# Kernel tuning notes

Hardware: AMD Instinct MI355X
Metric: run time of the kernel (lower is better)

Reference implementation:

```python
import jax, jax.numpy as jnp
import numpy as np

N, M, E, F, OUT = 20000, 2048, 320000, 512, 2
HID = F // 2
NEG_ATT = 0.2   # leaky_relu slope inside HypergraphConv attention
NEG = 0.01      # default F.leaky_relu / nn.LeakyReLU slope
EPS = 1e-5      # GraphNorm eps


def setup_inputs() -> dict:
    key = jax.random.key(0)
    ks = jax.random.split(key, 12)
    nrm = lambda k, shape, s=0.05: (jax.random.normal(k, shape, jnp.float32) * s)
    row = jax.random.randint(ks[1], (E,), 0, N)
    col = jax.random.randint(ks[2], (E,), 0, M)
    return dict(
        x=nrm(ks[0], (N, F), 1.0),
        edge_index=jnp.stack([row, col]),                 # [2, E] int32
        edge_attr=nrm(ks[3], (M, F), 1.0),
        W1=nrm(ks[4], (F, F)), att1=nrm(ks[5], (2 * F,)), b1=jnp.zeros((F,), jnp.float32),
        W2=nrm(ks[6], (F, F)), att2=nrm(ks[7], (2 * F,)), b2=jnp.zeros((F,), jnp.float32),
        gn1_w=jnp.ones((F,), jnp.float32), gn1_b=jnp.zeros((F,), jnp.float32), gn1_ms=jnp.ones((F,), jnp.float32),
        gn2_w=jnp.ones((F,), jnp.float32), gn2_b=jnp.zeros((F,), jnp.float32), gn2_ms=jnp.ones((F,), jnp.float32),
        fc1_W=nrm(ks[8], (F, HID)), fc1_b=jnp.zeros((HID,), jnp.float32),
        fc2_W=nrm(ks[9], (F, HID)), fc2_b=jnp.zeros((HID,), jnp.float32),
        cls_W=nrm(ks[10], (HID, OUT)), cls_b=jnp.zeros((OUT,), jnp.float32),
    )


def _segsum(v, idx, n):
    return jax.ops.segment_sum(v, idx, num_segments=n)


def hypergraph_conv(x, edge_attr, row, col, W, att, bias):
    """PyG HypergraphConv, heads=1, use_attention=True, attention_mode='node'."""
    xl = x @ W                          # [N, F] node features after lin
    el = edge_attr @ W                  # [M, F] hyperedge features after lin
    # attention logits per incidence: (cat[x_i, e_j] * att).sum(-1)
    pre = xl[row] @ att[:F] + el[col] @ att[F:]           # [E]
    alpha = jax.nn.leaky_relu(pre, NEG_ATT)
    # softmax grouped by hyperedge (col)
    amax = jax.ops.segment_max(alpha, col, num_segments=M)
    amax = jnp.where(jnp.isfinite(amax), amax, 0.0)
    ex = jnp.exp(alpha - amax[col])
    denom = _segsum(ex, col, M)
    alpha = ex / jnp.maximum(denom, 1e-16)[col]           # [E]
    # degree normalizations (hyperedge_weight = 1)
    ones = jnp.ones((row.shape[0],), xl.dtype)
    deg_n = _segsum(ones, row, N)
    Dinv = jnp.where(deg_n > 0, 1.0 / deg_n, 0.0)         # [N]
    deg_e = _segsum(ones, col, M)
    Binv = jnp.where(deg_e > 0, 1.0 / deg_e, 0.0)         # [M]
    # propagate 1: nodes -> hyperedges
    edge_feat = _segsum((alpha * Binv[col])[:, None] * xl[row], col, M)   # [M, F]
    # propagate 2: hyperedges -> nodes
    out = _segsum((alpha * Dinv[row])[:, None] * edge_feat[col], row, N)  # [N, F]
    return out + bias


def graph_norm(x, w, b, ms):
    # single graph (batch=None): normalize over all nodes
    mean = x.mean(axis=0)
    out = x - ms * mean
    var = (out * out).mean(axis=0)
    return out / jnp.sqrt(var + EPS) * w + b


def reference(x, edge_index, edge_attr,
              W1, att1, b1, W2, att2, b2,
              gn1_w, gn1_b, gn1_ms, gn2_w, gn2_b, gn2_ms,
              fc1_W, fc1_b, fc2_W, fc2_b, cls_W, cls_b):
    row, col = edge_index[0], edge_index[1]
    h = hypergraph_conv(x, edge_attr, row, col, W1, att1, b1)
    h = jax.nn.leaky_relu(graph_norm(h, gn1_w, gn1_b, gn1_ms), NEG)
    out = jax.nn.leaky_relu(h @ fc1_W + fc1_b, NEG)
    h = hypergraph_conv(h, edge_attr, row, col, W2, att2, b2)
    h = jax.nn.leaky_relu(graph_norm(h, gn2_w, gn2_b, gn2_ms), NEG)
    out = out + jax.nn.leaky_relu(h @ fc2_W + fc2_b, NEG)
    logits = out @ cls_W + cls_b
    return logits
```

## Files before the change

### kernel.cpp

```cpp
#include <hip/hip_runtime.h>
#include <math.h>

#define FDIM 512
#define HIDDIM 256
#define HB 128
#define SCH 1024
#define LDSK 32

typedef __bf16 bf16x8 __attribute__((ext_vector_type(8)));
typedef float floatx4 __attribute__((ext_vector_type(4)));

__device__ __forceinline__ float lrelu(float x, float s) { return x >= 0.0f ? x : s * x; }

__device__ __forceinline__ float bf2f(unsigned int u) {
  union { float f; unsigned int i; } v; v.i = u << 16; return v.f;
}
__device__ __forceinline__ unsigned short f2bf(float f) {
  union { float f; unsigned int u; } v; v.f = f;
  unsigned int x = v.u;
  return (unsigned short)((x + 0x7fffu + ((x >> 16) & 1u)) >> 16);
}

__device__ __forceinline__ void async_copy16(const unsigned short* g, unsigned short* l) {
  __builtin_amdgcn_global_load_lds((const __attribute__((address_space(1))) unsigned int*)g,
                                   (__attribute__((address_space(3))) unsigned int*)l, 16, 0, 0);
}

__device__ __forceinline__ float waveReduceSum(float v) {
#pragma unroll
  for (int o = 32; o; o >>= 1) v += __shfl_down(v, o, 64);
  return v;
}

__device__ __forceinline__ float blockReduceSum256(float v) {
  __shared__ float sm[4];
  int lane = threadIdx.x & 63, w = threadIdx.x >> 6;
  v = waveReduceSum(v);
  __syncthreads();
  if (lane == 0) sm[w] = v;
  __syncthreads();
  return sm[0] + sm[1] + sm[2] + sm[3];
}

__device__ __forceinline__ float blockReduceMax256(float v) {
  __shared__ float sm[4];
  int lane = threadIdx.x & 63, w = threadIdx.x >> 6;
#pragma unroll
  for (int o = 32; o; o >>= 1) v = fmaxf(v, __shfl_down(v, o, 64));
  __syncthreads();
  if (lane == 0) sm[w] = v;
  __syncthreads();
  return fmaxf(fmaxf(sm[0], sm[1]), fmaxf(sm[2], sm[3]));
}

__global__ __launch_bounds__(256) void k_hist2(const int* __restrict__ row, const int* __restrict__ col,
                                               int* __restrict__ cnt_r, int* __restrict__ cnt_c,
                                               int E, int nchunk) {
  __shared__ int h[2048];
  int b = blockIdx.x, t = threadIdx.x;
  for (int i = t; i < 2048; i += 256) h[i] = 0;
  __syncthreads();
  int s = b * nchunk, e = min(E, s + nchunk);
  for (int j = s + t; j < e; j += 256) {
    atomicAdd(&h[col[j]], 1);
    atomicAdd(&cnt_r[row[j]], 1);
  }
  __syncthreads();
  for (int i = t; i < 2048; i += 256) {
    int v = h[i];
    if (v) atomicAdd(&cnt_c[i], v);
  }
}

__global__ __launch_bounds__(256) void k_scan_part(const int* __restrict__ cnt, int* __restrict__ off,
                                                   int* __restrict__ btot, int n) {
  int b = blockIdx.x, t = threadIdx.x;
  int base = b * SCH + t * 4;
  int v[4];
#pragma unroll
  for (int i = 0; i < 4; ++i) v[i] = (base + i < n) ? cnt[base + i] : 0;
  int s = v[0] + v[1] + v[2] + v[3];
  int lane = t & 63, w = t >> 6;
  int x = s;
#pragma unroll
  for (int o = 1; o < 64; o <<= 1) {
    int y = __shfl_up(x, o, 64);
    if (lane >= o) x += y;
  }
  __shared__ int ws[4];
  if (lane == 63) ws[w] = x;
  __syncthreads();
  int wpre = 0;
  for (int i = 0; i < w; ++i) wpre += ws[i];
  int run = wpre + x - s;
#pragma unroll
  for (int i = 0; i < 4; ++i) {
    if (base + i < n) off[base + i] = run;
    run += v[i];
  }
  if (t == 255) btot[b] = wpre + x;
}

__global__ __launch_bounds__(256) void k_scan_midcol(int* __restrict__ btot, int nb,
                                                     const int* __restrict__ cnt_c, int* __restrict__ off_c,
                                                     int* __restrict__ gcur) {
  int t = threadIdx.x, lane = t & 63, w = t >> 6;
  __shared__ int ws[4];
  if (blockIdx.x == 0) {
    int v = (t < nb) ? btot[t] : 0;
    int x = v;
#pragma unroll
    for (int o = 1; o < 64; o <<= 1) {
      int y = __shfl_up(x, o, 64);
      if (lane >= o) x += y;
    }
    if (lane == 63) ws[w] = x;
    __syncthreads();
    int wpre = 0;
    for (int i = 0; i < w; ++i) wpre += ws[i];
    if (t < nb) btot[t] = wpre + x - v;
    if (t == 255) btot[nb] = wpre + x;
  } else {
    int base = t * 8;
    int v[8];
#pragma unroll
    for (int i = 0; i < 8; ++i) v[i] = cnt_c[base + i];
    int s = 0;
#pragma unroll
    for (int i = 0; i < 8; ++i) s += v[i];
    int x = s;
#pragma unroll
    for (int o = 1; o < 64; o <<= 1) {
      int y = __shfl_up(x, o, 64);
      if (lane >= o) x += y;
    }
    if (lane == 63) ws[w] = x;
    __syncthreads();
    int wpre = 0;
    for (int i = 0; i < w; ++i) wpre += ws[i];
    int run = wpre + x - s;
#pragma unroll
    for (int i = 0; i < 8; ++i) {
      off_c[base + i] = run;
      gcur[base + i] = run;
      run += v[i];
    }
    if (t == 255) off_c[2048] = wpre + x;
  }
}

__global__ __launch_bounds__(256) void k_scan_add(int* __restrict__ off, const int* __restrict__ btot,
                                                  int n, int nb) {
  int b = blockIdx.x, t = threadIdx.x;
  int base = b * SCH + t * 4;
  int add = btot[b];
#pragma unroll
  for (int i = 0; i < 4; ++i)
    if (base + i < n) off[base + i] += add;
  if (b == 0 && t == 0) off[n] = btot[nb];
}

__global__ __launch_bounds__(256) void k_fill3(const int* __restrict__ row, const int* __restrict__ col,
                                               int* __restrict__ gcur, const int* __restrict__ off_r,
                                               int* __restrict__ cur_r, int* __restrict__ prj,
                                               int* __restrict__ rj, int* __restrict__ cj,
                                               int E, int nchunk) {
  __shared__ int h[2048];
  __shared__ int lbase[2048];
  int b = blockIdx.x, t = threadIdx.x;
  for (int i = t; i < 2048; i += 256) h[i] = 0;
  __syncthreads();
  int s = b * nchunk, e = min(E, s + nchunk);
  for (int j = s + t; j < e; j += 256) atomicAdd(&h[col[j]], 1);
  __syncthreads();
  for (int i = t; i < 2048; i += 256) {
    int c = h[i];
    lbase[i] = c ? atomicAdd(&gcur[i], c) : 0;
    h[i] = 0;
  }
  __syncthreads();
  for (int j = s + t; j < e; j += 256) {
    int r = row[j], c = col[j];
    int slot_c = lbase[c] + atomicAdd(&h[c], 1);
    int slot_r = off_r[r] + atomicAdd(&cur_r[r], 1);
    rj[slot_c] = r;
    prj[slot_c] = slot_r;
    cj[slot_r] = c;
  }
}

__global__ __launch_bounds__(256) void k_hi(const float* __restrict__ A, unsigned short* __restrict__ hi, int n4) {
  int i = blockIdx.x * 256 + threadIdx.x;
  if (i < n4) {
    float4 v = ((const float4*)A)[i];
    ushort4 h;
    h.x = f2bf(v.x); h.y = f2bf(v.y); h.z = f2bf(v.z); h.w = f2bf(v.w);
    ((ushort4*)hi)[i] = h;
  }
}

__global__ __launch_bounds__(256) void k_prep_w_hi2(const float* __restrict__ W1, unsigned short* __restrict__ t1,
                                                    const float* __restrict__ W2, unsigned short* __restrict__ t2,
                                                    int K, int Nc) {
  const float* W = blockIdx.z ? W2 : W1;
  unsigned short* th = blockIdx.z ? t2 : t1;
  int n = blockIdx.x * 16 + (threadIdx.x & 15);
  int k = blockIdx.y * 16 + (threadIdx.x >> 4);
  th[(size_t)n * K + k] = f2bf(W[(size_t)k * Nc + n]);
}

__global__ __launch_bounds__(256) void k_prep_w2(const float* __restrict__ Wa, unsigned short* __restrict__ tha,
                                                 unsigned short* __restrict__ tla, const float* __restrict__ Wb,
                                                 unsigned short* __restrict__ thb, unsigned short* __restrict__ tlb,
                                                 int K, int Nc) {
  const float* W = blockIdx.z ? Wb : Wa;
  unsigned short* th = blockIdx.z ? thb : tha;
  unsigned short* tl = blockIdx.z ? tlb : tla;
  int n = blockIdx.x * 16 + (threadIdx.x & 15);
  int k = blockIdx.y * 16 + (threadIdx.x >> 4);
  float v = W[(size_t)k * Nc + n];
  unsigned short h = f2bf(v);
  unsigned short l = f2bf(v - bf2f(h));
  th[(size_t)n * K + k] = h;
  tl[(size_t)n * K + k] = l;
}

__global__ __launch_bounds__(256) void k_wv2(const float* __restrict__ W1, const float* __restrict__ a1,
                                             const float* __restrict__ W2, const float* __restrict__ a2,
                                             float* __restrict__ wv1, float* __restrict__ wv2) {
  int lane = threadIdx.x & 63, w = threadIdx.x >> 6;
  int k = blockIdx.x * 4 + w;
  const float* W = blockIdx.y ? W2 : W1;
  const float* a = blockIdx.y ? a2 : a1;
  float* wv = blockIdx.y ? wv2 : wv1;
  float s = 0.f;
  for (int f = lane; f < FDIM; f += 64) s = fmaf(W[(size_t)k * FDIM + f], a[f], s);
  s = waveReduceSum(s);
  if (lane == 0) wv[k] = s;
}

__global__ __launch_bounds__(256) void k_ea2(const float* __restrict__ X, const float* __restrict__ wv1,
                                             const float* __restrict__ wv2, float* __restrict__ ea1,
                                             float* __restrict__ ea2, int Mr) {
  int lane = threadIdx.x & 63, w = threadIdx.x >> 6;
  int m = blockIdx.x * 4 + w;
  if (m < Mr) {
    float s1 = 0.f, s2 = 0.f;
    for (int f = lane; f < FDIM; f += 64) {
      float v = X[(size_t)m * FDIM + f];
      s1 = fmaf(v, wv1[f], s1);
      s2 = fmaf(v, wv2[f], s2);
    }
    s1 = waveReduceSum(s1);
    s2 = waveReduceSum(s2);
    if (lane == 0) { ea1[m] = s1; ea2[m] = s2; }
  }
}

__device__ __forceinline__ bool xcd_decode(int id, int nP, int& panel, int& c) {
  panel = ((id >> 5) << 3) + (id & 7);
  c = (id >> 3) & 3;
  return panel < nP;
}

__global__ __launch_bounds__(256, 1) void gemm_conv(const unsigned short* __restrict__ Ah,
                                                    const unsigned short* __restrict__ Bth,
                                                    unsigned short* __restrict__ Cb,
                                                    const float* __restrict__ att, float* __restrict__ xa,
                                                    int Mr, int K, int Nc, int nP) {
  int panel, cblk;
  if (!xcd_decode(blockIdx.x, nP, panel, cblk)) return;
  __shared__ unsigned short lds[2 * 128 * LDSK];
  int tid = threadIdx.x, lane = tid & 63, w = tid >> 6;
  int wr = w >> 1, wc = w & 1;
  int rowB = panel * 128, colB = cblk * 128;

  const unsigned short* src = (w < 2) ? Ah : Bth;
  int baseRow = ((w < 2) ? rowB : colB) + 64 * (w & 1);
  int maxRow = (w < 2) ? (Mr - 1) : (Nc - 1);
  int slr = lane >> 2, slc = lane & 3;
  unsigned short* dstBase = &lds[((w >> 1) * 128 + (w & 1) * 64) * LDSK];

  size_t gro[4];
#pragma unroll
  for (int seg = 0; seg < 4; ++seg) {
    int rg = baseRow + seg * 16 + slr;
    if (rg > maxRow) rg = maxRow;
    gro[seg] = (size_t)rg * K + slc * 8;
  }

  floatx4 zero4 = {0.f, 0.f, 0.f, 0.f};
  floatx4 acc[4][4];
#pragma unroll
  for (int i = 0; i < 4; ++i)
#pragma unroll
    for (int j = 0; j < 4; ++j) acc[i][j] = zero4;

  int fr = lane & 15, fq = lane >> 4;
  int offA = (wr * 64 + fr) * LDSK + fq * 8;
  int offB = 128 * LDSK + (wc * 64 + fr) * LDSK + fq * 8;

  for (int k0 = 0; k0 < K; k0 += 32) {
#pragma unroll
    for (int seg = 0; seg < 4; ++seg) async_copy16(src + gro[seg] + k0, dstBase + seg * 16 * LDSK);
    __syncthreads();
    bf16x8 a[4], b[4];
#pragma unroll
    for (int t = 0; t < 4; ++t) {
      a[t] = *(const bf16x8*)(&lds[offA + t * 16 * LDSK]);
      b[t] = *(const bf16x8*)(&lds[offB + t * 16 * LDSK]);
    }
#pragma unroll
    for (int ti = 0; ti < 4; ++ti)
#pragma unroll
      for (int tj = 0; tj < 4; ++tj)
        acc[ti][tj] = __builtin_amdgcn_mfma_f32_16x16x32_bf16(a[ti], b[tj], acc[ti][tj], 0, 0, 0);
    __syncthreads();
  }

  int colL = colB + wc * 64 + fr;
  int rowL = rowB + wr * 64 + fq * 4;
  float attv[4];
#pragma unroll
  for (int tj = 0; tj < 4; ++tj) attv[tj] = att[colL + tj * 16];
#pragma unroll
  for (int ti = 0; ti < 4; ++ti) {
#pragma unroll
    for (int r = 0; r < 4; ++r) {
      int rr = rowL + ti * 16 + r;
      if (rr < Mr) {
        float dot = 0.f;
#pragma unroll
        for (int tj = 0; tj < 4; ++tj) {
          float v = acc[ti][tj][r];
          Cb[(size_t)rr * Nc + colL + tj * 16] = f2bf(v);
          dot = fmaf(v, attv[tj], dot);
        }
#pragma unroll
        for (int o = 1; o < 16; o <<= 1) dot += __shfl_xor(dot, o, 64);
        if ((lane & 15) == 0) atomicAdd(&xa[rr], dot);
      }
    }
  }
}

__global__ __launch_bounds__(256, 1) void gemm_fc_cls(const unsigned short* __restrict__ A1,
                                                      const unsigned short* __restrict__ B1h,
                                                      const unsigned short* __restrict__ B1l,
                                                      const float* __restrict__ b1,
                                                      const unsigned short* __restrict__ A2,
                                                      const unsigned short* __restrict__ B2h,
                                                      const unsigned short* __restrict__ B2l,
                                                      const float* __restrict__ b2,
                                                      const float* __restrict__ clsW, const float* __restrict__ clsb,
                                                      float* __restrict__ logits, int Mr, int K, int nP) {
  int panel, cblk;
  if (!xcd_decode(blockIdx.x, nP, panel, cblk)) return;
  __shared__ unsigned short lds[(128 + 2 * 64) * LDSK];
  int tid = threadIdx.x, lane = tid & 63, w = tid >> 6;
  int wr = w >> 1, wc = w & 1;
  int rowB = panel * 128, colB = cblk * 64;

  int slr = lane >> 2, slc = lane & 3;
  int baseRow = (w < 2) ? (rowB + 64 * w) : colB;
  int maxRow = (w < 2) ? (Mr - 1) : (HIDDIM - 1);
  unsigned short* dstBase = &lds[w * 64 * LDSK];

  size_t gro[4];
#pragma unroll
  for (int seg = 0; seg < 4; ++seg) {
    int rg = baseRow + seg * 16 + slr;
    if (rg > maxRow) rg = maxRow;
    gro[seg] = (size_t)rg * K + slc * 8;
  }

  int fr = lane & 15, fq = lane >> 4;
  int offA = (wr * 64 + fr) * LDSK + fq * 8;
  int offBh = (128 + wc * 32 + fr) * LDSK + fq * 8;
  int offBl = offBh + 64 * LDSK;

  floatx4 zero4 = {0.f, 0.f, 0.f, 0.f};
  floatx4 acc1[4][2], acc2[4][2];
#pragma unroll
  for (int i = 0; i < 4; ++i) {
    acc1[i][0] = zero4; acc1[i][1] = zero4;
    acc2[i][0] = zero4; acc2[i][1] = zero4;
  }

#pragma unroll
  for (int L = 0; L < 2; ++L) {
    const unsigned short* src =
        (L == 0) ? ((w < 2) ? A1 : (w == 2) ? B1h : B1l)
                 : ((w < 2) ? A2 : (w == 2) ? B2h : B2l);
    for (int k0 = 0; k0 < K; k0 += 32) {
#pragma unroll
      for (int seg = 0; seg < 4; ++seg) async_copy16(src + gro[seg] + k0, dstBase + seg * 16 * LDSK);
      __syncthreads();
      bf16x8 a[4], bh[2], bl[2];
#pragma unroll
      for (int t = 0; t < 4; ++t) a[t] = *(const bf16x8*)(&lds[offA + t * 16 * LDSK]);
#pragma unroll
      for (int t = 0; t < 2; ++t) {
        bh[t] = *(const bf16x8*)(&lds[offBh + t * 16 * LDSK]);
        bl[t] = *(const bf16x8*)(&lds[offBl + t * 16 * LDSK]);
      }
      if (L == 0) {
#pragma unroll
        for (int ti = 0; ti < 4; ++ti)
#pragma unroll
          for (int tj = 0; tj < 2; ++tj) {
            acc1[ti][tj] = __builtin_amdgcn_mfma_f32_16x16x32_bf16(a[ti], bh[tj], acc1[ti][tj], 0, 0, 0);
            acc1[ti][tj] = __builtin_amdgcn_mfma_f32_16x16x32_bf16(a[ti], bl[tj], acc1[ti][tj], 0, 0, 0);
          }
      } else {
#pragma unroll
        for (int ti = 0; ti < 4; ++ti)
#pragma unroll
          for (int tj = 0; tj < 2; ++tj) {
            acc2[ti][tj] = __builtin_amdgcn_mfma_f32_16x16x32_bf16(a[ti], bh[tj], acc2[ti][tj], 0, 0, 0);
            acc2[ti][tj] = __builtin_amdgcn_mfma_f32_16x16x32_bf16(a[ti], bl[tj], acc2[ti][tj], 0, 0, 0);
          }
      }
      __syncthreads();
    }
  }

  int colL = colB + wc * 32 + fr;
  int rowL = rowB + wr * 64 + fq * 4;
  float cw0[2], cw1[2], bb1[2], bb2[2];
#pragma unroll
  for (int tj = 0; tj < 2; ++tj) {
    int c = colL + tj * 16;
    cw0[tj] = clsW[2 * c];
    cw1[tj] = clsW[2 * c + 1];
    bb1[tj] = b1[c];
    bb2[tj] = b2[c];
  }
  bool addBias = (cblk == 0 && wc == 0);
  float cb0 = clsb[0], cb1 = clsb[1];
#pragma unroll
  for (int ti = 0; ti < 4; ++ti) {
#pragma unroll
    for (int r = 0; r < 4; ++r) {
      int rr = rowL + ti * 16 + r;
      if (rr < Mr) {
        float d0 = 0.f, d1 = 0.f;
#pragma unroll
        for (int tj = 0; tj < 2; ++tj) {
          float v = lrelu(acc1[ti][tj][r] + bb1[tj], 0.01f) + lrelu(acc2[ti][tj][r] + bb2[tj], 0.01f);
          d0 = fmaf(v, cw0[tj], d0);
          d1 = fmaf(v, cw1[tj], d1);
        }
#pragma unroll
        for (int o = 1; o < 16; o <<= 1) {
          d0 += __shfl_xor(d0, o, 64);
          d1 += __shfl_xor(d1, o, 64);
        }
        if ((lane & 15) == 0) {
          if (addBias) { d0 += cb0; d1 += cb1; }
          atomicAdd(&logits[2 * (size_t)rr], d0);
          atomicAdd(&logits[2 * (size_t)rr + 1], d1);
        }
      }
    }
  }
}

__global__ __launch_bounds__(256) void k_prop_col_f(const unsigned short* __restrict__ xl,
                                                    const float* __restrict__ xa, const float* __restrict__ ea,
                                                    const int* __restrict__ rj, const int* __restrict__ prj,
                                                    const int* __restrict__ off_c,
                                                    float* __restrict__ arj, unsigned short* __restrict__ ef) {
  int m = blockIdx.x;
  int s = off_c[m], e_ = off_c[m + 1];
  int cnt = e_ - s;
  float eam = ea[m];
  int t = threadIdx.x, lane = t & 63, w = t >> 6;

  __shared__ int sidx[512];
  __shared__ float swgt[512];
  __shared__ float pf[4][512];
  float acc[8] = {0, 0, 0, 0, 0, 0, 0, 0};

  if (cnt <= 512) {
    float mx = -3.402823466e38f;
    for (int j = t; j < cnt; j += 256) {
      int r = rj[s + j];
      float lg = lrelu(xa[r] + eam, 0.2f);
      sidx[j] = r;
      swgt[j] = lg;
      mx = fmaxf(mx, lg);
    }
    mx = blockReduceMax256(mx);
    float sum = 0.f;
    for (int j = t; j < cnt; j += 256) sum += expf(swgt[j] - mx);
    sum = blockReduceSum256(sum);
    float inv = 1.0f / fmaxf(sum, 1e-16f);
    for (int j = t; j < cnt; j += 256) {
      float a = expf(swgt[j] - mx) * inv;
      swgt[j] = a;
      arj[prj[s + j]] = a;
    }
    __syncthreads();
    int j = w;
    for (; j + 16 <= cnt; j += 16) {
      int r0 = sidx[j], r1 = sidx[j + 4], r2 = sidx[j + 8], r3 = sidx[j + 12];
      float w0 = swgt[j], w1 = swgt[j + 4], w2 = swgt[j + 8], w3 = swgt[j + 12];
      bf16x8 v0 = *(const bf16x8*)(xl + (size_t)r0 * FDIM + lane * 8);
      bf16x8 v1 = *(const bf16x8*)(xl + (size_t)r1 * FDIM + lane * 8);
      bf16x8 v2 = *(const bf16x8*)(xl + (size_t)r2 * FDIM + lane * 8);
      bf16x8 v3 = *(const bf16x8*)(xl + (size_t)r3 * FDIM + lane * 8);
#pragma unroll
      for (int i = 0; i < 8; ++i) acc[i] = fmaf(w0, (float)v0[i], acc[i]);
#pragma unroll
      for (int i = 0; i < 8; ++i) acc[i] = fmaf(w1, (float)v1[i], acc[i]);
#pragma unroll
      for (int i = 0; i < 8; ++i) acc[i] = fmaf(w2, (float)v2[i], acc[i]);
#pragma unroll
      for (int i = 0; i < 8; ++i) acc[i] = fmaf(w3, (float)v3[i], acc[i]);
    }
    for (; j < cnt; j += 4) {
      int r = sidx[j];
      float wt = swgt[j];
      bf16x8 v = *(const bf16x8*)(xl + (size_t)r * FDIM + lane * 8);
#pragma unroll
      for (int i = 0; i < 8; ++i) acc[i] = fmaf(wt, (float)v[i], acc[i]);
    }
    __syncthreads();
  } else {
    float mx = -3.402823466e38f;
    for (int j = s + t; j < e_; j += 256) mx = fmaxf(mx, lrelu(xa[rj[j]] + eam, 0.2f));
    mx = blockReduceMax256(mx);
    float sum = 0.f;
    for (int j = s + t; j < e_; j += 256) sum += expf(lrelu(xa[rj[j]] + eam, 0.2f) - mx);
    sum = blockReduceSum256(sum);
    float inv = 1.0f / fmaxf(sum, 1e-16f);
    for (int base = 0; base < cnt; base += 512) {
      int n = min(512, cnt - base);
      for (int j = t; j < n; j += 256) {
        int g = s + base + j;
        int r = rj[g];
        float a = expf(lrelu(xa[r] + eam, 0.2f) - mx) * inv;
        sidx[j] = r;
        swgt[j] = a;
        arj[prj[g]] = a;
      }
      __syncthreads();
      int j = w;
      for (; j + 4 <= n; j += 4) {
        int r = sidx[j];
        float wt = swgt[j];
        bf16x8 v = *(const bf16x8*)(xl + (size_t)r * FDIM + lane * 8);
#pragma unroll
        for (int i = 0; i < 8; ++i) acc[i] = fmaf(wt, (float)v[i], acc[i]);
      }
      if (j < n) {
        int r = sidx[j];
        float wt = swgt[j];
        bf16x8 v = *(const bf16x8*)(xl + (size_t)r * FDIM + lane * 8);
#pragma unroll
        for (int i = 0; i < 8; ++i) acc[i] = fmaf(wt, (float)v[i], acc[i]);
      }
      __syncthreads();
    }
  }

  float binv = cnt > 0 ? 1.0f / (float)cnt : 0.0f;
#pragma unroll
  for (int i = 0; i < 8; i += 2) *(float2*)&pf[w][lane * 8 + i] = make_float2(acc[i] * binv, acc[i + 1] * binv);
  __syncthreads();
  float2 r0 = ((const float2*)pf[0])[t], r1 = ((const float2*)pf[1])[t];
  float2 r2 = ((const float2*)pf[2])[t], r3 = ((const float2*)pf[3])[t];
  float a0 = r0.x + r1.x + r2.x + r3.x;
  float a1 = r0.y + r1.y + r2.y + r3.y;
  unsigned int o = (unsigned int)f2bf(a0) | ((unsigned int)f2bf(a1) << 16);
  ((unsigned int*)(ef + (size_t)m * FDIM))[t] = o;
}

__global__ __launch_bounds__(256) void k_prop_row(const unsigned short* __restrict__ ef,
                                                  const float* __restrict__ arj, const int* __restrict__ cj,
                                                  const int* __restrict__ off_r, const float* __restrict__ bias,
                                                  unsigned short* __restrict__ hb) {
  int nB = blockIdx.x;
  int s = off_r[nB], e_ = off_r[nB + 1];
  int cnt = e_ - s;
  __shared__ int sidx[512];
  __shared__ float swgt[512];
  __shared__ float pf[4][512];
  int t = threadIdx.x, lane = t & 63, w = t >> 6;
  float acc[8] = {0, 0, 0, 0, 0, 0, 0, 0};
  for (int base = 0; base < cnt; base += 512) {
    int n = min(512, cnt - base);
    for (int j = t; j < n; j += 256) {
      sidx[j] = cj[s + base + j];
      swgt[j] = arj[s + base + j];
    }
    __syncthreads();
    int j = w;
    for (; j + 8 <= n; j += 8) {
      int r0 = sidx[j], r1 = sidx[j + 4];
      float w0 = swgt[j], w1 = swgt[j + 4];
      bf16x8 v0 = *(const bf16x8*)(ef + (size_t)r0 * FDIM + lane * 8);
      bf16x8 v1 = *(const bf16x8*)(ef + (size_t)r1 * FDIM + lane * 8);
#pragma unroll
      for (int i = 0; i < 8; ++i) acc[i] = fmaf(w0, (float)v0[i], acc[i]);
#pragma unroll
      for (int i = 0; i < 8; ++i) acc[i] = fmaf(w1, (float)v1[i], acc[i]);
    }
    for (; j < n; j += 4) {
      int r = sidx[j];
      float wt = swgt[j];
      bf16x8 v = *(const bf16x8*)(ef + (size_t)r * FDIM + lane * 8);
#pragma unroll
      for (int i = 0; i < 8; ++i) acc[i] = fmaf(wt, (float)v[i], acc[i]);
    }
    __syncthreads();
  }
  float dinv = cnt > 0 ? 1.0f / (float)cnt : 0.0f;
#pragma unroll
  for (int i = 0; i < 8; i += 2) *(float2*)&pf[w][lane * 8 + i] = make_float2(acc[i] * dinv, acc[i + 1] * dinv);
  __syncthreads();
  float2 r0 = ((const float2*)pf[0])[t], r1 = ((const float2*)pf[1])[t];
  float2 r2 = ((const float2*)pf[2])[t], r3 = ((const float2*)pf[3])[t];
  float a0 = r0.x + r1.x + r2.x + r3.x + bias[2 * t];
  float a1 = r0.y + r1.y + r2.y + r3.y + bias[2 * t + 1];
  unsigned int o = (unsigned int)f2bf(a0) | ((unsigned int)f2bf(a1) << 16);
  ((unsigned int*)(hb + (size_t)nB * FDIM))[t] = o;
}

__global__ __launch_bounds__(256) void k_stats(const unsigned short* __restrict__ hb, float* __restrict__ gsum,
                                               float* __restrict__ gsq, int N) {
  int t = threadIdx.x;
  float s0 = 0, q0 = 0, s1 = 0, q1 = 0;
  for (int r = blockIdx.x; r < N; r += gridDim.x) {
    unsigned int u = ((const unsigned int*)(hb + (size_t)r * FDIM))[t];
    float v0 = bf2f(u & 0xffffu), v1 = bf2f(u >> 16);
    s0 += v0; q0 = fmaf(v0, v0, q0);
    s1 += v1; q1 = fmaf(v1, v1, q1);
  }
  atomicAdd(&gsum[2 * t], s0);
  atomicAdd(&gsq[2 * t], q0);
  atomicAdd(&gsum[2 * t + 1], s1);
  atomicAdd(&gsq[2 * t + 1], q1);
}

__global__ __launch_bounds__(256) void k_napply(const unsigned short* __restrict__ hb,
                                                const float* __restrict__ gsum, const float* __restrict__ gsq,
                                                const float* __restrict__ ms, const float* __restrict__ wg,
                                                const float* __restrict__ b, unsigned short* __restrict__ hi,
                                                float invn, int total2) {
  int i = blockIdx.x * 256 + threadIdx.x;
  if (i < total2) {
    int f2 = i & 255;
    int f0 = 2 * f2, f1 = 2 * f2 + 1;
    float mean0 = gsum[f0] * invn, mean1 = gsum[f1] * invn;
    float m0 = ms[f0], m1 = ms[f1];
    float var0 = gsq[f0] * invn - (2.0f * m0 - m0 * m0) * mean0 * mean0;
    float var1 = gsq[f1] * invn - (2.0f * m1 - m1 * m1) * mean1 * mean1;
    float scl0 = wg[f0] * __frsqrt_rn(var0 + 1e-5f);
    float scl1 = wg[f1] * __frsqrt_rn(var1 + 1e-5f);
    unsigned int u = ((const unsigned int*)hb)[i];
    float v0 = bf2f(u & 0xffffu), v1 = bf2f(u >> 16);
    v0 = lrelu((v0 - m0 * mean0) * scl0 + b[f0], 0.01f);
    v1 = lrelu((v1 - m1 * mean1) * scl1 + b[f1], 0.01f);
    ((unsigned int*)hi)[i] = (unsigned int)f2bf(v0) | ((unsigned int)f2bf(v1) << 16);
  }
}

extern "C" void kernel_launch(void* const* d_in, const int* in_sizes, int n_in,
                              void* d_out, int out_size, void* d_ws, size_t ws_size,
                              hipStream_t stream) {
  const float* x      = (const float*)d_in[0];
  const int*   eidx   = (const int*)d_in[1];
  const float* eattr  = (const float*)d_in[2];
  const float* W1     = (const float*)d_in[3];
  const float* att1   = (const float*)d_in[4];
  const float* b1     = (const float*)d_in[5];
  const float* W2     = (const float*)d_in[6];
  const float* att2   = (const float*)d_in[7];
  const float* b2     = (const float*)d_in[8];
  const float* gn1_w  = (const float*)d_in[9];
  const float* gn1_b  = (const float*)d_in[10];
  const float* gn1_ms = (const float*)d_in[11];
  const float* gn2_w  = (const float*)d_in[12];
  const float* gn2_b  = (const float*)d_in[13];
  const float* gn2_ms = (const float*)d_in[14];
  const float* fc1_W  = (const float*)d_in[15];
  const float* fc1_b  = (const float*)d_in[16];
  const float* fc2_W  = (const float*)d_in[17];
  const float* fc2_b  = (const float*)d_in[18];
  const float* cls_W  = (const float*)d_in[19];
  const float* cls_b  = (const float*)d_in[20];
  float* logits = (float*)d_out;

  const int N = in_sizes[0] / FDIM;
  const int E = in_sizes[1] / 2;
  const int M = in_sizes[2] / FDIM;
  const int* row = eidx;
  const int* col = eidx + E;
  const size_t NS = (size_t)N * FDIM;
  const size_t MS = (size_t)M * FDIM;

  char* base = (char*)d_ws;
  auto alloc = [&](size_t bytes) { char* r = base; base += (bytes + 255) & ~(size_t)255; return r; };

  unsigned short* xhi = (unsigned short*)alloc(NS * 2);
  unsigned short* xh1 = (unsigned short*)alloc(NS * 2);
  unsigned short* xh2 = (unsigned short*)alloc(NS * 2);
  unsigned short* xl  = (unsigned short*)alloc(NS * 2);
  unsigned short* hb  = (unsigned short*)alloc(NS * 2);
  unsigned short* ef  = (unsigned short*)alloc(MS * 2);
  unsigned short* w1th = (unsigned short*)alloc(FDIM * FDIM * 2);
  unsigned short* w2th = (unsigned short*)alloc(FDIM * FDIM * 2);
  unsigned short* f1th = (unsigned short*)alloc(FDIM * HIDDIM * 2);
  unsigned short* f1tl = (unsigned short*)alloc(FDIM * HIDDIM * 2);
  unsigned short* f2th = (unsigned short*)alloc(FDIM * HIDDIM * 2);
  unsigned short* f2tl = (unsigned short*)alloc(FDIM * HIDDIM * 2);
  float* wv1 = (float*)alloc(FDIM * 4);
  float* wv2 = (float*)alloc(FDIM * 4);
  float* ea1 = (float*)alloc((size_t)M * 4);
  float* ea2 = (float*)alloc((size_t)M * 4);
  float* arj = (float*)alloc((size_t)E * 4);
  int* off_r = (int*)alloc((size_t)(N + 1) * 4);
  int* off_c = (int*)alloc((size_t)(M + 1) * 4);
  int* gcur  = (int*)alloc((size_t)M * 4);
  int* rj    = (int*)alloc((size_t)E * 4);
  int* cj    = (int*)alloc((size_t)E * 4);
  int* prj   = (int*)alloc((size_t)E * 4);
  int* btot  = (int*)alloc(512 * 4);

  char* zstart = base;
  int* cnt_r = (int*)alloc((size_t)(2 * N + M) * 4);
  int* cur_r = cnt_r + N;
  int* cnt_c = cur_r + N;
  float* xa1 = (float*)alloc((size_t)N * 4);
  float* xa2 = (float*)alloc((size_t)N * 4);
  float* gsum1 = (float*)alloc(FDIM * 4);
  float* gsq1  = (float*)alloc(FDIM * 4);
  float* gsum2 = (float*)alloc(FDIM * 4);
  float* gsq2  = (float*)alloc(FDIM * 4);
  size_t zlen = (size_t)(base - zstart);
  hipMemsetAsync(zstart, 0, zlen, stream);
  hipMemsetAsync(logits, 0, (size_t)N * 2 * sizeof(float), stream);

  int nchunk = (E + HB - 1) / HB;
  int nbR = (N + SCH - 1) / SCH;
  k_hist2<<<HB, 256, 0, stream>>>(row, col, cnt_r, cnt_c, E, nchunk);
  k_scan_part<<<nbR, 256, 0, stream>>>(cnt_r, off_r, btot, N);
  k_scan_midcol<<<2, 256, 0, stream>>>(btot, nbR, cnt_c, off_c, gcur);
  k_scan_add<<<nbR, 256, 0, stream>>>(off_r, btot, N, nbR);
  k_fill3<<<HB, 256, 0, stream>>>(row, col, gcur, off_r, cur_r, prj, rj, cj, E, nchunk);

  k_hi<<<(int)((NS / 4 + 255) / 256), 256, 0, stream>>>(x, xhi, (int)(NS / 4));
  k_prep_w_hi2<<<dim3(FDIM / 16, FDIM / 16, 2), 256, 0, stream>>>(W1, w1th, W2, w2th, FDIM, FDIM);
  k_prep_w2<<<dim3(HIDDIM / 16, FDIM / 16, 2), 256, 0, stream>>>(fc1_W, f1th, f1tl, fc2_W, f2th, f2tl, FDIM, HIDDIM);
  k_wv2<<<dim3(FDIM / 4, 2), 256, 0, stream>>>(W1, att1 + FDIM, W2, att2 + FDIM, wv1, wv2);
  k_ea2<<<(M + 3) / 4, 256, 0, stream>>>(eattr, wv1, wv2, ea1, ea2, M);

  int gN128 = (N + 127) / 128;
  int nPpad4 = ((gN128 + 7) / 8) * 8 * 4;
  int napply_grid = (int)((NS / 2 + 255) / 256);
  float invn = 1.0f / (float)N;

  gemm_conv<<<nPpad4, 256, 0, stream>>>(xhi, w1th, xl, att1, xa1, N, FDIM, FDIM, gN128);
  k_prop_col_f<<<M, 256, 0, stream>>>(xl, xa1, ea1, rj, prj, off_c, arj, ef);
  k_prop_row<<<N, 256, 0, stream>>>(ef, arj, cj, off_r, b1, hb);
  k_stats<<<256, 256, 0, stream>>>(hb, gsum1, gsq1, N);
  k_napply<<<napply_grid, 256, 0, stream>>>(hb, gsum1, gsq1, gn1_ms, gn1_w, gn1_b, xh1, invn, (int)(NS / 2));

  gemm_conv<<<nPpad4, 256, 0, stream>>>(xh1, w2th, xl, att2, xa2, N, FDIM, FDIM, gN128);
  k_prop_col_f<<<M, 256, 0, stream>>>(xl, xa2, ea2, rj, prj, off_c, arj, ef);
  k_prop_row<<<N, 256, 0, stream>>>(ef, arj, cj, off_r, b2, hb);
  k_stats<<<256, 256, 0, stream>>>(hb, gsum2, gsq2, N);
  k_napply<<<napply_grid, 256, 0, stream>>>(hb, gsum2, gsq2, gn2_ms, gn2_w, gn2_b, xh2, invn, (int)(NS / 2));

  gemm_fc_cls<<<nPpad4, 256, 0, stream>>>(xh1, f1th, f1tl, fc1_b,
                                          xh2, f2th, f2tl, fc2_b,
                                          cls_W, cls_b, logits, N, FDIM, gN128);
}
```

Baseline: 527.3 us.

## Split hypergraph propagation kernels across two feature halves per segment

Both propagation kernels now launch two blocks per hyperedge or node, each handling 256 of the 512 feature columns with 4-wide bf16 loads. Block ids are interleaved in groups of eight so the two halves of a segment run close together. The goal is more parallelism and smaller per-block work, which should help load balance and latency hiding for the skewed degree distribution. The cost is that the column kernel's softmax, index and weight loading is done twice per hyperedge, and each gathered row access is half as wide.

After: 561.1 us. 1.06x slower.

```diff
diff --git a/kernel.cpp b/kernel.cpp
--- a/kernel.cpp
+++ b/kernel.cpp
@@ -8,6 +8,7 @@
 #define LDSK 32
 
 typedef __bf16 bf16x8 __attribute__((ext_vector_type(8)));
+typedef __bf16 bf16x4 __attribute__((ext_vector_type(4)));
 typedef float floatx4 __attribute__((ext_vector_type(4)));
 
 __device__ __forceinline__ float lrelu(float x, float s) { return x >= 0.0f ? x : s * x; }
@@ -470,17 +471,23 @@
                                                     const float* __restrict__ xa, const float* __restrict__ ea,
                                                     const int* __restrict__ rj, const int* __restrict__ prj,
                                                     const int* __restrict__ off_c,
-                                                    float* __restrict__ arj, unsigned short* __restrict__ ef) {
-  int m = blockIdx.x;
+                                                    float* __restrict__ arj, unsigned short* __restrict__ ef,
+                                                    int M) {
+  int id = blockIdx.x;
+  int xq = id & 7;
+  int half = xq >> 2;
+  int m = ((id >> 3) << 2) + (xq & 3);
+  if (m >= M) return;
   int s = off_c[m], e_ = off_c[m + 1];
   int cnt = e_ - s;
   float eam = ea[m];
   int t = threadIdx.x, lane = t & 63, w = t >> 6;
+  const unsigned short* xh = xl + half * 256;
 
   __shared__ int sidx[512];
   __shared__ float swgt[512];
-  __shared__ float pf[4][512];
-  float acc[8] = {0, 0, 0, 0, 0, 0, 0, 0};
+  __shared__ float pf[4][256];
+  float acc[4] = {0, 0, 0, 0};
 
   if (cnt <= 512) {
     float mx = -3.402823466e38f;
@@ -499,32 +506,32 @@
     for (int j = t; j < cnt; j += 256) {
       float a = expf(swgt[j] - mx) * inv;
       swgt[j] = a;
-      arj[prj[s + j]] = a;
+      if (half == 0) arj[prj[s + j]] = a;
     }
     __syncthreads();
     int j = w;
     for (; j + 16 <= cnt; j += 16) {
       int r0 = sidx[j], r1 = sidx[j + 4], r2 = sidx[j + 8], r3 = sidx[j + 12];
       float w0 = swgt[j], w1 = swgt[j + 4], w2 = swgt[j + 8], w3 = swgt[j + 12];
-      bf16x8 v0 = *(const bf16x8*)(xl + (size_t)r0 * FDIM + lane * 8);
-      bf16x8 v1 = *(const bf16x8*)(xl + (size_t)r1 * FDIM + lane * 8);
-      bf16x8 v2 = *(const bf16x8*)(xl + (size_t)r2 * FDIM + lane * 8);
-      bf16x8 v3 = *(const bf16x8*)(xl + (size_t)r3 * FDIM + lane * 8);
-#pragma unroll
-      for (int i = 0; i < 8; ++i) acc[i] = fmaf(w0, (float)v0[i], acc[i]);
-#pragma unroll
-      for (int i = 0; i < 8; ++i) acc[i] = fmaf(w1, (float)v1[i], acc[i]);
-#pragma unroll
-      for (int i = 0; i < 8; ++i) acc[i] = fmaf(w2, (float)v2[i], acc[i]);
-#pragma unroll
-      for (int i = 0; i < 8; ++i) acc[i] = fmaf(w3, (float)v3[i], acc[i]);
+      bf16x4 v0 = *(const bf16x4*)(xh + (size_t)r0 * FDIM + lane * 4);
+      bf16x4 v1 = *(const bf16x4*)(xh + (size_t)r1 * FDIM + lane * 4);
+      bf16x4 v2 = *(const bf16x4*)(xh + (size_t)r2 * FDIM + lane * 4);
+      bf16x4 v3 = *(const bf16x4*)(xh + (size_t)r3 * FDIM + lane * 4);
+#pragma unroll
+      for (int i = 0; i < 4; ++i) acc[i] = fmaf(w0, (float)v0[i], acc[i]);
+#pragma unroll
+      for (int i = 0; i < 4; ++i) acc[i] = fmaf(w1, (float)v1[i], acc[i]);
+#pragma unroll
+      for (int i = 0; i < 4; ++i) acc[i] = fmaf(w2, (float)v2[i], acc[i]);
+#pragma unroll
+      for (int i = 0; i < 4; ++i) acc[i] = fmaf(w3, (float)v3[i], acc[i]);
     }
     for (; j < cnt; j += 4) {
       int r = sidx[j];
       float wt = swgt[j];
-      bf16x8 v = *(const bf16x8*)(xl + (size_t)r * FDIM + lane * 8);
-#pragma unroll
-      for (int i = 0; i < 8; ++i) acc[i] = fmaf(wt, (float)v[i], acc[i]);
+      bf16x4 v = *(const bf16x4*)(xh + (size_t)r * FDIM + lane * 4);
+#pragma unroll
+      for (int i = 0; i < 4; ++i) acc[i] = fmaf(wt, (float)v[i], acc[i]);
     }
     __syncthreads();
   } else {
@@ -543,23 +550,15 @@
         float a = expf(lrelu(xa[r] + eam, 0.2f) - mx) * inv;
         sidx[j] = r;
         swgt[j] = a;
-        arj[prj[g]] = a;
+        if (half == 0) arj[prj[g]] = a;
       }
       __syncthreads();
-      int j = w;
-      for (; j + 4 <= n; j += 4) {
+      for (int j = w; j < n; j += 4) {
         int r = sidx[j];
         float wt = swgt[j];
-        bf16x8 v = *(const bf16x8*)(xl + (size_t)r * FDIM + lane * 8);
-#pragma unroll
-        for (int i = 0; i < 8; ++i) acc[i] = fmaf(wt, (float)v[i], acc[i]);
-      }
-      if (j < n) {
-        int r = sidx[j];
-        float wt = swgt[j];
-        bf16x8 v = *(const bf16x8*)(xl + (size_t)r * FDIM + lane * 8);
-#pragma unroll
-        for (int i = 0; i < 8; ++i) acc[i] = fmaf(wt, (float)v[i], acc[i]);
+        bf16x4 v = *(const bf16x4*)(xh + (size_t)r * FDIM + lane * 4);
+#pragma unroll
+        for (int i = 0; i < 4; ++i) acc[i] = fmaf(wt, (float)v[i], acc[i]);
       }
       __syncthreads();
     }
@@ -567,28 +566,29 @@
 
   float binv = cnt > 0 ? 1.0f / (float)cnt : 0.0f;
 #pragma unroll
-  for (int i = 0; i < 8; i += 2) *(float2*)&pf[w][lane * 8 + i] = make_float2(acc[i] * binv, acc[i + 1] * binv);
-  __syncthreads();
-  float2 r0 = ((const float2*)pf[0])[t], r1 = ((const float2*)pf[1])[t];
-  float2 r2 = ((const float2*)pf[2])[t], r3 = ((const float2*)pf[3])[t];
-  float a0 = r0.x + r1.x + r2.x + r3.x;
-  float a1 = r0.y + r1.y + r2.y + r3.y;
-  unsigned int o = (unsigned int)f2bf(a0) | ((unsigned int)f2bf(a1) << 16);
-  ((unsigned int*)(ef + (size_t)m * FDIM))[t] = o;
+  for (int i = 0; i < 4; ++i) pf[w][lane * 4 + i] = acc[i] * binv;
+  __syncthreads();
+  float v = pf[0][t] + pf[1][t] + pf[2][t] + pf[3][t];
+  ef[(size_t)m * FDIM + half * 256 + t] = f2bf(v);
 }
 
 __global__ __launch_bounds__(256) void k_prop_row(const unsigned short* __restrict__ ef,
                                                   const float* __restrict__ arj, const int* __restrict__ cj,
                                                   const int* __restrict__ off_r, const float* __restrict__ bias,
-                                                  unsigned short* __restrict__ hb) {
-  int nB = blockIdx.x;
+                                                  unsigned short* __restrict__ hb, int N) {
+  int id = blockIdx.x;
+  int xq = id & 7;
+  int half = xq >> 2;
+  int nB = ((id >> 3) << 2) + (xq & 3);
+  if (nB >= N) return;
   int s = off_r[nB], e_ = off_r[nB + 1];
   int cnt = e_ - s;
+  const unsigned short* eh = ef + half * 256;
   __shared__ int sidx[512];
   __shared__ float swgt[512];
-  __shared__ float pf[4][512];
+  __shared__ float pf[4][256];
   int t = threadIdx.x, lane = t & 63, w = t >> 6;
-  float acc[8] = {0, 0, 0, 0, 0, 0, 0, 0};
+  float acc[4] = {0, 0, 0, 0};
   for (int base = 0; base < cnt; base += 512) {
     int n = min(512, cnt - base);
     for (int j = t; j < n; j += 256) {
@@ -597,35 +597,38 @@
     }
     __syncthreads();
     int j = w;
-    for (; j + 8 <= n; j += 8) {
-      int r0 = sidx[j], r1 = sidx[j + 4];
-      float w0 = swgt[j], w1 = swgt[j + 4];
-      bf16x8 v0 = *(const bf16x8*)(ef + (size_t)r0 * FDIM + lane * 8);
-      bf16x8 v1 = *(const bf16x8*)(ef + (size_t)r1 * FDIM + lane * 8);
-#pragma unroll
-      for (int i = 0; i < 8; ++i) acc[i] = fmaf(w0, (float)v0[i], acc[i]);
-#pragma unroll
-      for (int i = 0; i < 8; ++i) acc[i] = fmaf(w1, (float)v1[i], acc[i]);
+    for (; j + 16 <= n; j += 16) {
+      int r0 = sidx[j], r1 = sidx[j + 4], r2 = sidx[j + 8], r3 = sidx[j + 12];
+      float w0 = swgt[j], w1 = swgt[j + 4], w2 = swgt[j + 8], w3 = swgt[j + 12];
+      bf16x4 v0 = *(const bf16x4*)(eh + (size_t)r0 * FDIM + lane * 4);
+      bf16x4 v1 = *(const bf16x4*)(eh + (size_t)r1 * FDIM + lane * 4);
+      bf16x4 v2 = *(const bf16x4*)(eh + (size_t)r2 * FDIM + lane * 4);
+      bf16x4 v3 = *(const bf16x4*)(eh + (size_t)r3 * FDIM + lane * 4);
+#pragma unroll
+      for (int i = 0; i < 4; ++i) acc[i] = fmaf(w0, (float)v0[i], acc[i]);
+#pragma unroll
+      for (int i = 0; i < 4; ++i) acc[i] = fmaf(w1, (float)v1[i], acc[i]);
+#pragma unroll
+      for (int i = 0; i < 4; ++i) acc[i] = fmaf(w2, (float)v2[i], acc[i]);
+#pragma unroll
+      for (int i = 0; i < 4; ++i) acc[i] = fmaf(w3, (float)v3[i], acc[i]);
     }
     for (; j < n; j += 4) {
       int r = sidx[j];
       float wt = swgt[j];
-      bf16x8 v = *(const bf16x8*)(ef + (size_t)r * FDIM + lane * 8);
-#pragma unroll
-      for (int i = 0; i < 8; ++i) acc[i] = fmaf(wt, (float)v[i], acc[i]);
+      bf16x4 v = *(const bf16x4*)(eh + (size_t)r * FDIM + lane * 4);
+#pragma unroll
+      for (int i = 0; i < 4; ++i) acc[i] = fmaf(wt, (float)v[i], acc[i]);
     }
     __syncthreads();
   }
   float dinv = cnt > 0 ? 1.0f / (float)cnt : 0.0f;
 #pragma unroll
-  for (int i = 0; i < 8; i += 2) *(float2*)&pf[w][lane * 8 + i] = make_float2(acc[i] * dinv, acc[i + 1] * dinv);
-  __syncthreads();
-  float2 r0 = ((const float2*)pf[0])[t], r1 = ((const float2*)pf[1])[t];
-  float2 r2 = ((const float2*)pf[2])[t], r3 = ((const float2*)pf[3])[t];
-  float a0 = r0.x + r1.x + r2.x + r3.x + bias[2 * t];
-  float a1 = r0.y + r1.y + r2.y + r3.y + bias[2 * t + 1];
-  unsigned int o = (unsigned int)f2bf(a0) | ((unsigned int)f2bf(a1) << 16);
-  ((unsigned int*)(hb + (size_t)nB * FDIM))[t] = o;
+  for (int i = 0; i < 4; ++i) pf[w][lane * 4 + i] = acc[i] * dinv;
+  __syncthreads();
+  int f = half * 256 + t;
+  float v = pf[0][t] + pf[1][t] + pf[2][t] + pf[3][t] + bias[f];
+  hb[(size_t)nB * FDIM + f] = f2bf(v);
 }
 
 __global__ __launch_bounds__(256) void k_stats(const unsigned short* __restrict__ hb, float* __restrict__ gsum,
@@ -759,18 +762,20 @@
 
   int gN128 = (N + 127) / 128;
   int nPpad4 = ((gN128 + 7) / 8) * 8 * 4;
+  int gPC = ((M + 3) / 4) * 8;
+  int gPR = ((N + 3) / 4) * 8;
   int napply_grid = (int)((NS / 2 + 255) / 256);
   float invn = 1.0f / (float)N;
 
   gemm_conv<<<nPpad4, 256, 0, stream>>>(xhi, w1th, xl, att1, xa1, N, FDIM, FDIM, gN128);
-  k_prop_col_f<<<M, 256, 0, stream>>>(xl, xa1, ea1, rj, prj, off_c, arj, ef);
-  k_prop_row<<<N, 256, 0, stream>>>(ef, arj, cj, off_r, b1, hb);
+  k_prop_col_f<<<gPC, 256, 0, stream>>>(xl, xa1, ea1, rj, prj, off_c, arj, ef, M);
+  k_prop_row<<<gPR, 256, 0, stream>>>(ef, arj, cj, off_r, b1, hb, N);
   k_stats<<<256, 256, 0, stream>>>(hb, gsum1, gsq1, N);
   k_napply<<<napply_grid, 256, 0, stream>>>(hb, gsum1, gsq1, gn1_ms, gn1_w, gn1_b, xh1, invn, (int)(NS / 2));
 
   gemm_conv<<<nPpad4, 256, 0, stream>>>(xh1, w2th, xl, att2, xa2, N, FDIM, FDIM, gN128);
-  k_prop_col_f<<<M, 256, 0, stream>>>(xl, xa2, ea2, rj, prj, off_c, arj, ef);
-  k_prop_row<<<N, 256, 0, stream>>>(ef, arj, cj, off_r, b2, hb);
+  k_prop_col_f<<<gPC, 256, 0, stream>>>(xl, xa2, ea2, rj, prj, off_c, arj, ef, M);
+  k_prop_row<<<gPR, 256, 0, stream>>>(ef, arj, cj, off_r, b2, hb, N);
   k_stats<<<256, 256, 0, stream>>>(hb, gsum2, gsq2, N);
   k_napply<<<napply_grid, 256, 0, stream>>>(hb, gsum2, gsq2, gn2_ms, gn2_w, gn2_b, xh2, invn, (int)(NS / 2));
 
```
